# Kernel optimization log

Measured on AMD Instinct MI355X. Metric: run time of the kernel, lower is better.

Reference implementation:

```python
import jax, jax.numpy as jnp
import numpy as np

N_QUBITS = 4
Q_DEPTH = 6
Q_DELTA = 0.01
BATCH = 65536


def _apply_ry(state, theta, q):
    """Apply RY(theta) on qubit q. state: [B,2,2,2,2]; theta: [B] (per-sample) or scalar.
    RY = [[cos(t/2), -sin(t/2)], [sin(t/2), cos(t/2)]] (PennyLane convention, real)."""
    c = jnp.cos(theta * 0.5)
    s = jnp.sin(theta * 0.5)
    s0 = jnp.take(state, 0, axis=q + 1)  # [B,2,2,2]
    s1 = jnp.take(state, 1, axis=q + 1)
    if jnp.ndim(theta) == 1:  # per-sample angle -> broadcast over remaining qubit axes
        c = c[:, None, None, None]
        s = s[:, None, None, None]
    new0 = c * s0 - s * s1
    new1 = s * s0 + c * s1
    return jnp.stack([new0, new1], axis=q + 1)


def _cnot(state, ctrl, tgt):
    """CNOT with control `ctrl`, target `tgt` on state [B,2,2,2,2]."""
    s0 = jnp.take(state, 0, axis=ctrl + 1)
    s1 = jnp.take(state, 1, axis=ctrl + 1)
    # target axis index inside the reduced (rank-4) array
    t_ax = tgt + 1 if tgt < ctrl else tgt
    s1 = jnp.flip(s1, axis=t_ax)
    return jnp.stack([s0, s1], axis=ctrl + 1)


def quantum_circuit(q_in, q_params):
    """Batched 4-qubit variational circuit. q_in: [B,4], q_params: [24].
    Circuit is real-valued (H, RY, CNOT on |0...0>), so state is float."""
    B = q_in.shape[0]
    # H layer on |0000> -> uniform amplitude 1/4 over all 16 basis states
    state = jnp.full((B, 2, 2, 2, 2), 0.25, dtype=q_in.dtype)
    for q in range(N_QUBITS):
        state = _apply_ry(state, q_in[:, q], q)
    qw = q_params.reshape(Q_DEPTH, N_QUBITS)
    for k in range(Q_DEPTH):
        # entangling layer: CNOT(0,1), CNOT(2,3), then CNOT(1,2)
        state = _cnot(state, 0, 1)
        state = _cnot(state, 2, 3)
        state = _cnot(state, 1, 2)
        for q in range(N_QUBITS):
            state = _apply_ry(state, qw[k, q], q)
    probs = state * state  # [B,2,2,2,2]
    zs = []
    for q in range(N_QUBITS):
        other = tuple(a for a in (1, 2, 3, 4) if a != q + 1)
        m = probs.sum(axis=other)  # [B,2]
        zs.append(m[:, 0] - m[:, 1])  # <Z_q> = P(0) - P(1)
    return jnp.stack(zs, axis=1)  # [B,4]


def setup_inputs() -> dict:
    key = jax.random.key(0)
    k1, k2, k3, k4 = jax.random.split(key, 4)
    return {
        "input_features": jax.random.normal(k1, (BATCH, 512), dtype=jnp.float32),
        "W_pre": jax.random.normal(k2, (N_QUBITS, 512), dtype=jnp.float32) * (1.0 / np.sqrt(512.0)),
        "b_pre": jnp.zeros((N_QUBITS,), dtype=jnp.float32),
        "q_params": Q_DELTA * jax.random.normal(k3, (Q_DEPTH * N_QUBITS,), dtype=jnp.float32),
        "W_post": jax.random.normal(k4, (200, N_QUBITS), dtype=jnp.float32) * 0.5,
        "b_post": jnp.zeros((200,), dtype=jnp.float32),
    }


def reference(input_features, W_pre, b_pre, q_params, W_post, b_post):
    pre_out = input_features @ W_pre.T + b_pre          # [B,4]
    q_in = jnp.tanh(pre_out) * (np.pi / 2.0)            # scale to (-pi/2, pi/2)
    q_out = quantum_circuit(q_in, q_params)             # [B,4]
    return q_out @ W_post.T + b_post                    # [B,200]
```

## Files before the change

### kernel.cpp

```cpp
#include <hip/hip_runtime.h>


#define BLOCK 256
#define WS 4
#define SPB 16

typedef float f4 __attribute__((ext_vector_type(4)));

__device__ __forceinline__ f4 ntload4(const float* p) {
  return __builtin_nontemporal_load((const f4*)p);
}

__device__ __forceinline__ float fast_tanh(float x) {
  const float e = __expf(2.0f * x);
  return 1.0f - 2.0f * __builtin_amdgcn_rcpf(e + 1.0f);
}

__device__ __forceinline__ float rs_step(float v0, float v1, bool hi, int m) {
  const float sd = hi ? v0 : v1;
  const float kp = hi ? v1 : v0;
  return kp + __shfl_xor(sd, m, 64);
}

template<int Q>
__device__ __forceinline__ void apply_ry(float (&st)[16], float c, float s) {
  constexpr int pos = 3 - Q;
  #pragma unroll
  for (int i = 0; i < 16; ++i) {
    if (((i >> pos) & 1) == 0) {
      const int j = i | (1 << pos);
      const float a = st[i], b = st[j];
      st[i] = c * a - s * b;
      st[j] = s * a + c * b;
    }
  }
}

template<int C, int T>
__device__ __forceinline__ void cnot(float (&st)[16]) {
  constexpr int pc = 3 - C, pt = 3 - T;
  #pragma unroll
  for (int i = 0; i < 16; ++i) {
    if ((((i >> pc) & 1) == 1) && (((i >> pt) & 1) == 0)) {
      const int j = i | (1 << pt);
      const float t = st[i]; st[i] = st[j]; st[j] = t;
    }
  }
}

__global__ __launch_bounds__(BLOCK, 4) void dqnet_kernel(
    const float* __restrict__ in, const float* __restrict__ Wpre,
    const float* __restrict__ bpre, const float* __restrict__ qp,
    const float* __restrict__ Wpost, const float* __restrict__ bpost,
    float* __restrict__ out) {
  __shared__ float s_wpost[200 * 4];
  __shared__ float s_bpost[200];
  __shared__ float s_c[24], s_sn[24];
  __shared__ f4 s_qout[SPB];

  const int tid = threadIdx.x;
  const int lane = tid & 63;
  const int wave = tid >> 6;

  if (tid < 200) {
    ((f4*)s_wpost)[tid] = ((const f4*)Wpost)[tid];
    s_bpost[tid] = bpost[tid];
  } else if (tid < 224) {
    const int k = tid - 200;
    const float a = qp[k] * 0.5f;
    s_c[k] = __cosf(a);
    s_sn[k] = __sinf(a);
  }

  f4 wa[4], wb[4];
  #pragma unroll
  for (int q = 0; q < 4; ++q) {
    wa[q] = *(const f4*)(Wpre + q * 512 + lane * 4);
    wb[q] = *(const f4*)(Wpre + q * 512 + 256 + lane * 4);
  }

  const int tile = blockIdx.x * SPB + wave * WS;
  const float* rb = in + (size_t)tile * 512 + lane * 4;

  const bool b1 = (lane & 1) != 0;
  const bool b2 = (lane & 2) != 0;

  float part[WS];
  f4 pxa[2], pxb[2];
  pxa[0] = ntload4(rb);        pxb[0] = ntload4(rb + 256);
  pxa[1] = ntload4(rb + 512);  pxb[1] = ntload4(rb + 512 + 256);
  #pragma unroll
  for (int s = 0; s < WS; ++s) {
    const f4 xa = pxa[s & 1], xb = pxb[s & 1];
    if (s + 2 < WS) {
      pxa[s & 1] = ntload4(rb + (size_t)(s + 2) * 512);
      pxb[s & 1] = ntload4(rb + (size_t)(s + 2) * 512 + 256);
    }
    float p0 = xa.x*wa[0].x + xa.y*wa[0].y + xa.z*wa[0].z + xa.w*wa[0].w
             + xb.x*wb[0].x + xb.y*wb[0].y + xb.z*wb[0].z + xb.w*wb[0].w;
    float p1 = xa.x*wa[1].x + xa.y*wa[1].y + xa.z*wa[1].z + xa.w*wa[1].w
             + xb.x*wb[1].x + xb.y*wb[1].y + xb.z*wb[1].z + xb.w*wb[1].w;
    float p2 = xa.x*wa[2].x + xa.y*wa[2].y + xa.z*wa[2].z + xa.w*wa[2].w
             + xb.x*wb[2].x + xb.y*wb[2].y + xb.z*wb[2].z + xb.w*wb[2].w;
    float p3 = xa.x*wa[3].x + xa.y*wa[3].y + xa.z*wa[3].z + xa.w*wa[3].w
             + xb.x*wb[3].x + xb.y*wb[3].y + xb.z*wb[3].z + xb.w*wb[3].w;
    const float a01 = rs_step(p0, p1, b1, 1);
    const float a23 = rs_step(p2, p3, b1, 1);
    part[s] = rs_step(a01, a23, b2, 2);
  }

  const bool b4 = (lane & 4) != 0;
  const bool b8 = (lane & 8) != 0;
  float a2[2];
  a2[0] = rs_step(part[0], part[1], b4, 4);
  a2[1] = rs_step(part[2], part[3], b4, 4);
  float r = rs_step(a2[0], a2[1], b8, 8);
  r += __shfl_xor(r, 16, 64);
  r += __shfl_xor(r, 32, 64);

  const float g0 = __shfl(r, (lane << 2) | 0, 64);
  const float g1 = __shfl(r, (lane << 2) | 1, 64);
  const float g2 = __shfl(r, (lane << 2) | 2, 64);
  const float g3 = __shfl(r, (lane << 2) | 3, 64);

  __syncthreads();

  if (lane < WS) {
    constexpr float PI_4 = 0.7853981633974483f;
    float c[4], sn[4], sv, cv;
    __sincosf(fast_tanh(g0 + bpre[0]) * PI_4, &sv, &cv); c[0] = cv; sn[0] = sv;
    __sincosf(fast_tanh(g1 + bpre[1]) * PI_4, &sv, &cv); c[1] = cv; sn[1] = sv;
    __sincosf(fast_tanh(g2 + bpre[2]) * PI_4, &sv, &cv); c[2] = cv; sn[2] = sv;
    __sincosf(fast_tanh(g3 + bpre[3]) * PI_4, &sv, &cv); c[3] = cv; sn[3] = sv;

    const float u0 = (c[0] - sn[0]) * 0.25f, v0 = (c[0] + sn[0]) * 0.25f;
    const float u1 =  c[1] - sn[1],          v1 =  c[1] + sn[1];
    const float u2 =  c[2] - sn[2],          v2 =  c[2] + sn[2];
    const float u3 =  c[3] - sn[3],          v3 =  c[3] + sn[3];
    const float thi[4] = {u0*u1, u0*v1, v0*u1, v0*v1};
    const float tlo[4] = {u2*u3, u2*v3, v2*u3, v2*v3};
    float st[16];
    #pragma unroll
    for (int i = 0; i < 16; ++i) st[i] = thi[i >> 2] * tlo[i & 3];

    #pragma unroll
    for (int k = 0; k < 6; ++k) {
      cnot<0,1>(st); cnot<2,3>(st); cnot<1,2>(st);
      apply_ry<0>(st, s_c[k*4+0], s_sn[k*4+0]);
      apply_ry<1>(st, s_c[k*4+1], s_sn[k*4+1]);
      apply_ry<2>(st, s_c[k*4+2], s_sn[k*4+2]);
      apply_ry<3>(st, s_c[k*4+3], s_sn[k*4+3]);
    }

    float p[16];
    #pragma unroll
    for (int i = 0; i < 16; ++i) p[i] = st[i] * st[i];
    float z0 = 0.f, z1 = 0.f, z2 = 0.f, z3 = 0.f;
    #pragma unroll
    for (int i = 0; i < 16; ++i) {
      z0 += ((i >> 3) & 1) ? -p[i] : p[i];
      z1 += ((i >> 2) & 1) ? -p[i] : p[i];
      z2 += ((i >> 1) & 1) ? -p[i] : p[i];
      z3 += ((i     ) & 1) ? -p[i] : p[i];
    }
    f4 z; z.x = z0; z.y = z1; z.z = z2; z.w = z3;
    s_qout[wave * WS + lane] = z;
  }
  __syncthreads();

  float* ob = out + (size_t)blockIdx.x * (SPB * 200);
  #pragma unroll
  for (int i = 0; i < 4; ++i) {
    const int idx4 = tid + i * BLOCK;
    if (idx4 < SPB * 50) {
      const int sloc = idx4 / 50;
      const int j4 = idx4 - sloc * 50;
      const f4 qo = s_qout[sloc];
      const f4* wrow = (const f4*)&s_wpost[j4 * 16];
      const float* br = &s_bpost[j4 * 4];
      f4 o;
      o.x = br[0] + wrow[0].x*qo.x + wrow[0].y*qo.y + wrow[0].z*qo.z + wrow[0].w*qo.w;
      o.y = br[1] + wrow[1].x*qo.x + wrow[1].y*qo.y + wrow[1].z*qo.z + wrow[1].w*qo.w;
      o.z = br[2] + wrow[2].x*qo.x + wrow[2].y*qo.y + wrow[2].z*qo.z + wrow[2].w*qo.w;
      o.w = br[3] + wrow[3].x*qo.x + wrow[3].y*qo.y + wrow[3].z*qo.z + wrow[3].w*qo.w;
      __builtin_nontemporal_store(o, (f4*)(ob + (size_t)idx4 * 4));
    }
  }
}

extern "C" void kernel_launch(void* const* d_in, const int* in_sizes, int n_in,
                              void* d_out, int out_size, void* d_ws, size_t ws_size,
                              hipStream_t stream) {
  const float* in    = (const float*)d_in[0];
  const float* Wpre  = (const float*)d_in[1];
  const float* bpre  = (const float*)d_in[2];
  const float* qp    = (const float*)d_in[3];
  const float* Wpost = (const float*)d_in[4];
  const float* bpost = (const float*)d_in[5];
  float* out = (float*)d_out;

  const int B = in_sizes[0] / 512;
  const int nblk = B / SPB;
  dqnet_kernel<<<nblk, BLOCK, 0, stream>>>(in, Wpre, bpre, qp, Wpost, bpost, out);
}
```

Measured before the change: 207.6 us.

## Distribute quantum state amplitudes across lanes using cross-lane shuffles

Replaces the per-sample serial 16-amplitude circuit simulation, run by only 4 lanes per wave, with a layout where each lane holds one amplitude (16 lanes per sample, 4 samples per wave). CNOT and RY gates become shuffle-xor exchanges with lane-bit selects, and the Z expectations come from a Walsh-style butterfly reduction. The aim is to stop 60 of 64 lanes idling during the circuit stage and to shorten that serial section. The cost is many dependent cross-lane shuffles.

```diff
diff --git a/kernel.cpp b/kernel.cpp
--- a/kernel.cpp
+++ b/kernel.cpp
@@ -22,32 +22,6 @@
   return kp + __shfl_xor(sd, m, 64);
 }
 
-template<int Q>
-__device__ __forceinline__ void apply_ry(float (&st)[16], float c, float s) {
-  constexpr int pos = 3 - Q;
-  #pragma unroll
-  for (int i = 0; i < 16; ++i) {
-    if (((i >> pos) & 1) == 0) {
-      const int j = i | (1 << pos);
-      const float a = st[i], b = st[j];
-      st[i] = c * a - s * b;
-      st[j] = s * a + c * b;
-    }
-  }
-}
-
-template<int C, int T>
-__device__ __forceinline__ void cnot(float (&st)[16]) {
-  constexpr int pc = 3 - C, pt = 3 - T;
-  #pragma unroll
-  for (int i = 0; i < 16; ++i) {
-    if ((((i >> pc) & 1) == 1) && (((i >> pt) & 1) == 0)) {
-      const int j = i | (1 << pt);
-      const float t = st[i]; st[i] = st[j]; st[j] = t;
-    }
-  }
-}
-
 __global__ __launch_bounds__(BLOCK, 4) void dqnet_kernel(
     const float* __restrict__ in, const float* __restrict__ Wpre,
     const float* __restrict__ bpre, const float* __restrict__ qp,
@@ -55,7 +29,7 @@
     float* __restrict__ out) {
   __shared__ float s_wpost[200 * 4];
   __shared__ float s_bpost[200];
-  __shared__ float s_c[24], s_sn[24];
+  __shared__ f4 s_c4[6], s_s4[6];
   __shared__ f4 s_qout[SPB];
 
   const int tid = threadIdx.x;
@@ -68,9 +42,11 @@
   } else if (tid < 224) {
     const int k = tid - 200;
     const float a = qp[k] * 0.5f;
-    s_c[k] = __cosf(a);
-    s_sn[k] = __sinf(a);
+    ((float*)s_c4)[k] = __cosf(a);
+    ((float*)s_s4)[k] = __sinf(a);
   }
+
+  const float bpre_a = bpre[lane & 3];
 
   f4 wa[4], wb[4];
   #pragma unroll
@@ -118,53 +94,61 @@
   r += __shfl_xor(r, 16, 64);
   r += __shfl_xor(r, 32, 64);
 
-  const float g0 = __shfl(r, (lane << 2) | 0, 64);
-  const float g1 = __shfl(r, (lane << 2) | 1, 64);
-  const float g2 = __shfl(r, (lane << 2) | 2, 64);
-  const float g3 = __shfl(r, (lane << 2) | 3, 64);
-
   __syncthreads();
 
-  if (lane < WS) {
-    constexpr float PI_4 = 0.7853981633974483f;
-    float c[4], sn[4], sv, cv;
-    __sincosf(fast_tanh(g0 + bpre[0]) * PI_4, &sv, &cv); c[0] = cv; sn[0] = sv;
-    __sincosf(fast_tanh(g1 + bpre[1]) * PI_4, &sv, &cv); c[1] = cv; sn[1] = sv;
-    __sincosf(fast_tanh(g2 + bpre[2]) * PI_4, &sv, &cv); c[2] = cv; sn[2] = sv;
-    __sincosf(fast_tanh(g3 + bpre[3]) * PI_4, &sv, &cv); c[3] = cv; sn[3] = sv;
+  const int g = lane >> 4;
+  const int a = lane & 15;
+  const bool bitp0 = (a & 1) != 0;
+  const bool bitp1 = (a & 2) != 0;
+  const bool bitp2 = (a & 4) != 0;
+  const bool bitp3 = (a & 8) != 0;
 
-    const float u0 = (c[0] - sn[0]) * 0.25f, v0 = (c[0] + sn[0]) * 0.25f;
-    const float u1 =  c[1] - sn[1],          v1 =  c[1] + sn[1];
-    const float u2 =  c[2] - sn[2],          v2 =  c[2] + sn[2];
-    const float u3 =  c[3] - sn[3],          v3 =  c[3] + sn[3];
-    const float thi[4] = {u0*u1, u0*v1, v0*u1, v0*v1};
-    const float tlo[4] = {u2*u3, u2*v3, v2*u3, v2*v3};
-    float st[16];
-    #pragma unroll
-    for (int i = 0; i < 16; ++i) st[i] = thi[i >> 2] * tlo[i & 3];
+  constexpr float PI_4 = 0.7853981633974483f;
+  const float rg = __shfl(r, (g << 2) | (a & 3), 64);
+  float sv, cv;
+  __sincosf(fast_tanh(rg + bpre_a) * PI_4, &sv, &cv);
 
-    #pragma unroll
-    for (int k = 0; k < 6; ++k) {
-      cnot<0,1>(st); cnot<2,3>(st); cnot<1,2>(st);
-      apply_ry<0>(st, s_c[k*4+0], s_sn[k*4+0]);
-      apply_ry<1>(st, s_c[k*4+1], s_sn[k*4+1]);
-      apply_ry<2>(st, s_c[k*4+2], s_sn[k*4+2]);
-      apply_ry<3>(st, s_c[k*4+3], s_sn[k*4+3]);
-    }
+  float cq[4], sq[4];
+  #pragma unroll
+  for (int q = 0; q < 4; ++q) {
+    const int src = (lane & 48) | q;
+    cq[q] = __shfl(cv, src, 64);
+    sq[q] = __shfl(sv, src, 64);
+  }
+  const float ss0 = bitp3 ? sq[0] : -sq[0];
+  const float ss1 = bitp2 ? sq[1] : -sq[1];
+  const float ss2 = bitp1 ? sq[2] : -sq[2];
+  const float ss3 = bitp0 ? sq[3] : -sq[3];
 
-    float p[16];
-    #pragma unroll
-    for (int i = 0; i < 16; ++i) p[i] = st[i] * st[i];
-    float z0 = 0.f, z1 = 0.f, z2 = 0.f, z3 = 0.f;
-    #pragma unroll
-    for (int i = 0; i < 16; ++i) {
-      z0 += ((i >> 3) & 1) ? -p[i] : p[i];
-      z1 += ((i >> 2) & 1) ? -p[i] : p[i];
-      z2 += ((i >> 1) & 1) ? -p[i] : p[i];
-      z3 += ((i     ) & 1) ? -p[i] : p[i];
-    }
-    f4 z; z.x = z0; z.y = z1; z.z = z2; z.w = z3;
-    s_qout[wave * WS + lane] = z;
+  float st = (cq[0] + ss0) * (cq[1] + ss1) * ((cq[2] + ss2) * (cq[3] + ss3))
+           * 0.25f;
+
+  #pragma unroll
+  for (int k = 0; k < 6; ++k) {
+    { const float pt = __shfl_xor(st, 4, 64); st = bitp3 ? pt : st; }
+    { const float pt = __shfl_xor(st, 1, 64); st = bitp1 ? pt : st; }
+    { const float pt = __shfl_xor(st, 2, 64); st = bitp2 ? pt : st; }
+    const f4 ck = s_c4[k];
+    const f4 sk = s_s4[k];
+    { const float pt = __shfl_xor(st, 8, 64);
+      st = ck.x * st + (bitp3 ? sk.x : -sk.x) * pt; }
+    { const float pt = __shfl_xor(st, 4, 64);
+      st = ck.y * st + (bitp2 ? sk.y : -sk.y) * pt; }
+    { const float pt = __shfl_xor(st, 2, 64);
+      st = ck.z * st + (bitp1 ? sk.z : -sk.z) * pt; }
+    { const float pt = __shfl_xor(st, 1, 64);
+      st = ck.w * st + (bitp0 ? sk.w : -sk.w) * pt; }
+  }
+
+  float pv = st * st;
+  { const float o = __shfl_xor(pv, 1, 64); pv = bitp0 ? (o - pv) : (pv + o); }
+  { const float o = __shfl_xor(pv, 2, 64); pv = bitp1 ? (o - pv) : (pv + o); }
+  { const float o = __shfl_xor(pv, 4, 64); pv = bitp2 ? (o - pv) : (pv + o); }
+  { const float o = __shfl_xor(pv, 8, 64); pv = bitp3 ? (o - pv) : (pv + o); }
+
+  if (__popc(a) == 1) {
+    const int q = 3 - __builtin_ctz(a);
+    ((float*)s_qout)[(wave * WS + g) * 4 + q] = pv;
   }
   __syncthreads();
 
```

Result: no change. 203.6 us (median of 2 runs) (-2.0%).
